# Optimization experiments

Measured on AMD Instinct MI355X. Metric: run time of the kernel, lower is better.

## Reference

```python
import jax, jax.numpy as jnp
import numpy as np

N_NODES = 50000
N_EDGES = 600000
IN_FEATS = 128
N_HIDDEN = 128
N_CLASSES = 40


def setup_inputs() -> dict:
    key = jax.random.key(0)
    ks = jax.random.split(key, 12)
    feat = jax.random.normal(ks[0], (N_NODES, IN_FEATS), dtype=jnp.float32)
    src = jax.random.randint(ks[1], (N_EDGES,), 0, N_NODES, dtype=jnp.int32)
    dst = jax.random.randint(ks[2], (N_EDGES,), 0, N_NODES, dtype=jnp.int32)
    dims = [(IN_FEATS, N_HIDDEN), (N_HIDDEN, N_HIDDEN), (N_HIDDEN, N_CLASSES)]
    params = {}
    for i, (di, do) in enumerate(dims):
        s = 1.0 / np.sqrt(di)
        params[f"w_self{i}"] = jax.random.uniform(ks[3 + 3 * i], (di, do), jnp.float32, -s, s)
        params[f"w_neigh{i}"] = jax.random.uniform(ks[4 + 3 * i], (di, do), jnp.float32, -s, s)
        params[f"b{i}"] = jnp.zeros((do,), jnp.float32)
    return dict(feat=feat, src=src, dst=dst, **params)


def _sage_layer(h, src, dst, w_self, w_neigh, b):
    # mean aggregation over in-neighbors: msg = h[src], reduce at dst
    msg_sum = jax.ops.segment_sum(h[src], dst, num_segments=N_NODES)  # [N, d]
    deg = jax.ops.segment_sum(jnp.ones((src.shape[0],), h.dtype), dst, num_segments=N_NODES)
    h_neigh = msg_sum / jnp.maximum(deg, 1.0)[:, None]
    # DGL SAGEConv(mean): out = fc_self(h) + fc_neigh(mean_neigh) + bias
    return h @ w_self + h_neigh @ w_neigh + b


def reference(feat, src, dst,
              w_self0, w_neigh0, b0,
              w_self1, w_neigh1, b1,
              w_self2, w_neigh2, b2):
    # dropout p=0.0 -> identity
    h = _sage_layer(feat, src, dst, w_self0, w_neigh0, b0)
    h = jax.nn.relu(h)
    h = _sage_layer(h, src, dst, w_self1, w_neigh1, b1)
    h = jax.nn.relu(h)
    h = _sage_layer(h, src, dst, w_self2, w_neigh2, b2)
    return h
```

## Files before the change

### kernel.cpp

```cpp
#include <hip/hip_runtime.h>

#define N_NODES 50000
#define N_EDGES 600000

typedef short bf16x8 __attribute__((ext_vector_type(8)));
typedef float f32x4  __attribute__((ext_vector_type(4)));
typedef unsigned short u16x8 __attribute__((ext_vector_type(8)));
typedef unsigned short u16x4 __attribute__((ext_vector_type(4)));

typedef __attribute__((address_space(1))) unsigned int u32_g;
typedef __attribute__((address_space(3))) unsigned int u32_l;

__device__ inline void g2lds16(const void* g, void* l) {
    __builtin_amdgcn_global_load_lds((const u32_g*)g, (u32_l*)l, 16, 0, 0);
}

__device__ inline ushort rne_bf16(float a) {
    union { float f; unsigned u; } v; v.f = a;
    return (ushort)((v.u + 0x7FFFu + ((v.u >> 16) & 1u)) >> 16);
}
__device__ inline float bf16_to_f32(ushort h) {
    return __uint_as_float((unsigned)h << 16);
}
__device__ inline void split_bf16(float a, ushort& hi, ushort& lo) {
    hi = rne_bf16(a);
    float hv = bf16_to_f32(hi);
    lo = rne_bf16(a - hv);
}


__global__ void count_deg_kernel(const int* __restrict__ dst, int* __restrict__ deg, int ne) {
    int e = blockIdx.x * blockDim.x + threadIdx.x;
    if (e < ne) atomicAdd(&deg[dst[e]], 1);
}

__global__ __launch_bounds__(256) void block_sums_kernel(const int* __restrict__ deg,
                                                         int* __restrict__ bsum, int n) {
    __shared__ int s[256];
    int t = threadIdx.x;
    int i = blockIdx.x * 256 + t;
    s[t] = (i < n) ? deg[i] : 0;
    __syncthreads();
    #pragma unroll
    for (int d = 128; d > 0; d >>= 1) {
        if (t < d) s[t] += s[t + d];
        __syncthreads();
    }
    if (t == 0) bsum[blockIdx.x] = s[0];
}

__global__ __launch_bounds__(256) void scan_bsums_kernel(const int* __restrict__ bsum,
                                                         int* __restrict__ base, int nb,
                                                         int* __restrict__ off, int n) {
    __shared__ int s[256];
    int t = threadIdx.x;
    int v = (t < nb) ? bsum[t] : 0;
    s[t] = v;
    __syncthreads();
    #pragma unroll
    for (int d = 1; d < 256; d <<= 1) {
        int x = (t >= d) ? s[t - d] : 0;
        __syncthreads();
        s[t] += x;
        __syncthreads();
    }
    if (t < nb) base[t] = s[t] - v;
    if (t == 255) off[n] = s[255];
}

__global__ __launch_bounds__(256) void scatter_offsets_kernel(const int* __restrict__ deg,
                                                              const int* __restrict__ base,
                                                              int* __restrict__ off,
                                                              int* __restrict__ cur, int n) {
    __shared__ int s[256];
    int t = threadIdx.x;
    int i = blockIdx.x * 256 + t;
    int v = (i < n) ? deg[i] : 0;
    s[t] = v;
    __syncthreads();
    #pragma unroll
    for (int d = 1; d < 256; d <<= 1) {
        int x = (t >= d) ? s[t - d] : 0;
        __syncthreads();
        s[t] += x;
        __syncthreads();
    }
    if (i < n) {
        int excl = s[t] - v + base[blockIdx.x];
        off[i] = excl;
        cur[i] = excl;
    }
}

__global__ void fill_csr_kernel(const int* __restrict__ src, const int* __restrict__ dst,
                                int* __restrict__ cur, int* __restrict__ ssrc, int ne) {
    int e = blockIdx.x * blockDim.x + threadIdx.x;
    if (e < ne) {
        int p = atomicAdd(&cur[dst[e]], 1);
        ssrc[p] = src[e];
    }
}

__global__ void convert_w_kernel(const float* __restrict__ Ws, const float* __restrict__ Wn,
                                 int dout, ushort* __restrict__ Bth, ushort* __restrict__ Btl) {
    int n = blockIdx.x;
    int k = threadIdx.x;
    float w = (n < dout) ? Ws[(long)k * dout + n] : Wn[(long)k * dout + (n - dout)];
    ushort hi, lo;
    split_bf16(w, hi, lo);
    Bth[n * 128 + k] = hi;
    Btl[n * 128 + k] = lo;
}

__global__ __launch_bounds__(256) void convert_feat_kernel(const float* __restrict__ A,
                                                           ushort* __restrict__ Ah,
                                                           ushort* __restrict__ Al) {
    long g = ((long)blockIdx.x * 256 + threadIdx.x) * 8;
    float4 a0 = *(const float4*)(A + g);
    float4 a1 = *(const float4*)(A + g + 4);
    float f[8] = {a0.x, a0.y, a0.z, a0.w, a1.x, a1.y, a1.z, a1.w};
    u16x8 h, l;
    #pragma unroll
    for (int i = 0; i < 8; ++i) {
        ushort hh, ll;
        split_bf16(f[i], hh, ll);
        h[i] = hh; l[i] = ll;
    }
    *(u16x8*)(Ah + g) = h;
    *(u16x8*)(Al + g) = l;
}


#define KDIM 128
#define TILES 3
#define RPB   (32 * TILES)

__global__ __launch_bounds__(512) void gemm_mfma_wide(
    const ushort* __restrict__ Ah, const ushort* __restrict__ Al,
    const ushort* __restrict__ Bth, const ushort* __restrict__ Btl,
    const float* __restrict__ bias,
    float* __restrict__ S, ushort* __restrict__ T, int M)
{
    __shared__ ushort AhL[32 * 128];
    __shared__ ushort AlL[32 * 128];

    const int tid = threadIdx.x;
    const int wave = tid >> 6;
    const int lane = tid & 63;
    const int lane16 = lane & 15;
    const int quad = lane >> 4;
    const int colbase = wave * 32;
    const int rowbase = blockIdx.x * RPB;

    bf16x8 bh[2][4], bl[2][4];
    #pragma unroll
    for (int ct = 0; ct < 2; ++ct) {
        #pragma unroll
        for (int c = 0; c < 4; ++c) {
            long boff = (long)(colbase + 16 * ct + lane16) * KDIM + c * 32 + quad * 8;
            bh[ct][c] = *(const bf16x8*)(Bth + boff);
            bl[ct][c] = *(const bf16x8*)(Btl + boff);
        }
    }

    const int srow = tid >> 4;
    const int su   = (tid & 15) ^ (srow & 15);
    const int lds_wave_off = wave * 512;

    for (int t = 0; t < TILES; ++t) {
        const int r0 = rowbase + t * 32;
        {
            const ushort* ga = Ah + ((long)(r0 + srow) * KDIM + su * 8);
            const ushort* gb = Al + ((long)(r0 + srow) * KDIM + su * 8);
            g2lds16(ga, (void*)(AhL + lds_wave_off));
            g2lds16(gb, (void*)(AlL + lds_wave_off));
        }
        __syncthreads();

        f32x4 acc[2][2] = {};
        #pragma unroll
        for (int c = 0; c < 4; ++c) {
            bf16x8 ah[2], al[2];
            #pragma unroll
            for (int rt = 0; rt < 2; ++rt) {
                int row = 16 * rt + lane16;
                int u = (4 * c + quad) ^ lane16;
                int offs = row * 128 + u * 8;
                ah[rt] = *(const bf16x8*)&AhL[offs];
                al[rt] = *(const bf16x8*)&AlL[offs];
            }
            #pragma unroll
            for (int ct = 0; ct < 2; ++ct)
                #pragma unroll
                for (int rt = 0; rt < 2; ++rt)
                    acc[rt][ct] = __builtin_amdgcn_mfma_f32_16x16x32_bf16(ah[rt], bh[ct][c], acc[rt][ct], 0, 0, 0);
            #pragma unroll
            for (int ct = 0; ct < 2; ++ct)
                #pragma unroll
                for (int rt = 0; rt < 2; ++rt)
                    acc[rt][ct] = __builtin_amdgcn_mfma_f32_16x16x32_bf16(ah[rt], bl[ct][c], acc[rt][ct], 0, 0, 0);
            #pragma unroll
            for (int ct = 0; ct < 2; ++ct)
                #pragma unroll
                for (int rt = 0; rt < 2; ++rt)
                    acc[rt][ct] = __builtin_amdgcn_mfma_f32_16x16x32_bf16(al[rt], bh[ct][c], acc[rt][ct], 0, 0, 0);
        }

        #pragma unroll
        for (int ct = 0; ct < 2; ++ct) {
            int col = colbase + 16 * ct + lane16;
            bool toS = col < 128;
            float bv = toS ? bias[col] : 0.f;
            int tcol = toS ? col : col - 128;
            #pragma unroll
            for (int rt = 0; rt < 2; ++rt) {
                #pragma unroll
                for (int i = 0; i < 4; ++i) {
                    int row = r0 + 16 * rt + quad * 4 + i;
                    if (row < M) {
                        if (toS) S[(long)row * 128 + tcol] = acc[rt][ct][i] + bv;
                        else     T[(long)row * 128 + tcol] = rne_bf16(acc[rt][ct][i]);
                    }
                }
            }
        }
        __syncthreads();
    }
}

__global__ __launch_bounds__(256) void gemm_mfma_narrow(
    const ushort* __restrict__ Ah, const ushort* __restrict__ Al,
    const ushort* __restrict__ Bth, const ushort* __restrict__ Btl,
    const float* __restrict__ bias,
    float* __restrict__ S, ushort* __restrict__ T, int M)
{
    const int tid = threadIdx.x;
    const int wave = tid >> 6;
    const int brow = blockIdx.x * 64 + wave * 16;
    const int lane = tid & 63;
    const int lane16 = lane & 15;
    const int quad = lane >> 4;

    f32x4 acc[5] = {};

    #pragma unroll
    for (int c = 0; c < 4; ++c) {
        const int k0 = c * 32;
        long aoff = (long)(brow + lane16) * KDIM + k0 + quad * 8;
        bf16x8 ah = *(const bf16x8*)(Ah + aoff);
        bf16x8 al = *(const bf16x8*)(Al + aoff);
        bf16x8 bh[5], bl[5];
        #pragma unroll
        for (int ct = 0; ct < 5; ++ct) {
            long boff = (long)(16 * ct + lane16) * KDIM + k0 + quad * 8;
            bh[ct] = *(const bf16x8*)(Bth + boff);
            bl[ct] = *(const bf16x8*)(Btl + boff);
        }
        #pragma unroll
        for (int ct = 0; ct < 5; ++ct)
            acc[ct] = __builtin_amdgcn_mfma_f32_16x16x32_bf16(ah, bh[ct], acc[ct], 0, 0, 0);
        #pragma unroll
        for (int ct = 0; ct < 5; ++ct)
            acc[ct] = __builtin_amdgcn_mfma_f32_16x16x32_bf16(ah, bl[ct], acc[ct], 0, 0, 0);
        #pragma unroll
        for (int ct = 0; ct < 5; ++ct)
            acc[ct] = __builtin_amdgcn_mfma_f32_16x16x32_bf16(al, bh[ct], acc[ct], 0, 0, 0);
    }

    #pragma unroll
    for (int ct = 0; ct < 5; ++ct) {
        int col = 16 * ct + lane16;
        bool toS = col < 40;
        float bv = toS ? bias[col] : 0.f;
        int tcol = toS ? col : col - 40;
        #pragma unroll
        for (int i = 0; i < 4; ++i) {
            int row = brow + quad * 4 + i;
            if (row < M) {
                if (toS) S[(long)row * 40 + tcol] = acc[ct][i] + bv;
                else     T[(long)row * 40 + tcol] = rne_bf16(acc[ct][i]);
            }
        }
    }
}


__global__ __launch_bounds__(256) void agg128_split_kernel(
    const float* __restrict__ S, const ushort* __restrict__ T,
    const int* __restrict__ off, const int* __restrict__ ssrc,
    ushort* __restrict__ Oh, ushort* __restrict__ Ol, int nnodes)
{
    const int node = (blockIdx.x * 256 + threadIdx.x) >> 6;
    if (node >= nnodes) return;
    const int lane = threadIdx.x & 63;
    const int slot = lane >> 4;
    const int col8 = (lane & 15) * 8;

    const int a = off[node];
    const int b = off[node + 1];

    f32x4 acc0a = {0,0,0,0}, acc0b = {0,0,0,0};
    f32x4 acc1a = {0,0,0,0}, acc1b = {0,0,0,0};

    int i = a;
    for (; i + 8 <= b; i += 8) {
        int s0 = ssrc[i + slot];
        int s1 = ssrc[i + 4 + slot];
        u16x8 v0 = *(const u16x8*)(T + (long)s0 * 128 + col8);
        u16x8 v1 = *(const u16x8*)(T + (long)s1 * 128 + col8);
        #pragma unroll
        for (int j = 0; j < 4; ++j) {
            acc0a[j] += bf16_to_f32(v0[j]);
            acc0b[j] += bf16_to_f32(v0[4 + j]);
            acc1a[j] += bf16_to_f32(v1[j]);
            acc1b[j] += bf16_to_f32(v1[4 + j]);
        }
    }
    for (; i < b; i += 4) {
        int e = i + slot;
        if (e < b) {
            int s = ssrc[e];
            u16x8 v = *(const u16x8*)(T + (long)s * 128 + col8);
            #pragma unroll
            for (int j = 0; j < 4; ++j) {
                acc0a[j] += bf16_to_f32(v[j]);
                acc0b[j] += bf16_to_f32(v[4 + j]);
            }
        }
    }
    f32x4 accA = acc0a + acc1a;
    f32x4 accB = acc0b + acc1b;

    #pragma unroll
    for (int m = 16; m <= 32; m <<= 1) {
        #pragma unroll
        for (int j = 0; j < 4; ++j) {
            accA[j] += __shfl_xor((float)accA[j], m);
            accB[j] += __shfl_xor((float)accB[j], m);
        }
    }

    if (slot == 0) {
        int deg = b - a;
        float scale = (deg > 0) ? (1.0f / (float)deg) : 0.f;
        f32x4 sA = *(const f32x4*)(S + (long)node * 128 + col8);
        f32x4 sB = *(const f32x4*)(S + (long)node * 128 + col8 + 4);
        float r[8];
        #pragma unroll
        for (int j = 0; j < 4; ++j) {
            r[j]     = fmaxf(sA[j] + accA[j] * scale, 0.f);
            r[4 + j] = fmaxf(sB[j] + accB[j] * scale, 0.f);
        }
        u16x8 h, l;
        #pragma unroll
        for (int j = 0; j < 8; ++j) {
            ushort hh, ll;
            split_bf16(r[j], hh, ll);
            h[j] = hh; l[j] = ll;
        }
        *(u16x8*)(Oh + (long)node * 128 + col8) = h;
        *(u16x8*)(Ol + (long)node * 128 + col8) = l;
    }
}

__global__ __launch_bounds__(256) void agg40_kernel(
    const float* __restrict__ S, const ushort* __restrict__ T,
    const int* __restrict__ off, const int* __restrict__ ssrc,
    float* __restrict__ out, int nnodes)
{
    const int node = (blockIdx.x * 256 + threadIdx.x) >> 6;
    if (node >= nnodes) return;
    const int lane = threadIdx.x & 63;
    const bool active = lane < 60;
    const int slot = active ? (lane / 10) : 5;
    const int fi = lane % 10;
    const int fo = fi * 4;

    const int a = off[node];
    const int b = off[node + 1];

    f32x4 acc0 = {0,0,0,0}, acc1 = {0,0,0,0};

    int i = a;
    for (; i + 12 <= b; i += 12) {
        int s0 = ssrc[i + slot];
        int s1 = ssrc[i + 6 + slot];
        u16x4 v0 = *(const u16x4*)(T + (long)s0 * 40 + fo);
        u16x4 v1 = *(const u16x4*)(T + (long)s1 * 40 + fo);
        if (active) {
            #pragma unroll
            for (int j = 0; j < 4; ++j) {
                acc0[j] += bf16_to_f32(v0[j]);
                acc1[j] += bf16_to_f32(v1[j]);
            }
        }
    }
    for (; i < b; i += 6) {
        int e = i + slot;
        if (active && e < b) {
            int s = ssrc[e];
            u16x4 v = *(const u16x4*)(T + (long)s * 40 + fo);
            #pragma unroll
            for (int j = 0; j < 4; ++j) acc0[j] += bf16_to_f32(v[j]);
        }
    }
    f32x4 acc = acc0 + acc1;

    f32x4 tot = acc;
    #pragma unroll
    for (int d = 10; d <= 50; d += 10) {
        int srcl = fi + d;
        #pragma unroll
        for (int j = 0; j < 4; ++j) tot[j] += __shfl((float)acc[j], srcl);
    }

    if (lane < 10) {
        int deg = b - a;
        float scale = (deg > 0) ? (1.0f / (float)deg) : 0.f;
        f32x4 s4 = *(const f32x4*)(S + (long)node * 40 + fo);
        f32x4 r = s4 + tot * scale;
        *(f32x4*)(out + (long)node * 40 + fo) = r;
    }
}


extern "C" void kernel_launch(void* const* d_in, const int* in_sizes, int n_in,
                              void* d_out, int out_size, void* d_ws, size_t ws_size,
                              hipStream_t stream) {
    const float* feat = (const float*)d_in[0];
    const int*   src  = (const int*)d_in[1];
    const int*   dst  = (const int*)d_in[2];
    const float* ws0  = (const float*)d_in[3];
    const float* wn0  = (const float*)d_in[4];
    const float* b0   = (const float*)d_in[5];
    const float* ws1  = (const float*)d_in[6];
    const float* wn1  = (const float*)d_in[7];
    const float* b1   = (const float*)d_in[8];
    const float* ws2  = (const float*)d_in[9];
    const float* wn2  = (const float*)d_in[10];
    const float* b2   = (const float*)d_in[11];

    const int N = N_NODES;
    const int NE = N_EDGES;
    const int NB = (N + 255) / 256;

    char* ws = (char*)d_ws;
    int*    offsets = (int*)(ws + 0);
    int*    cursor  = (int*)(ws + 200704);
    int*    degi    = (int*)(ws + 401408);
    int*    bsum    = (int*)(ws + 601600);
    int*    bbase   = (int*)(ws + 602432);
    int*    ssrc    = (int*)(ws + 603648);
    ushort* Bth0 = (ushort*)(ws + 200704);
    ushort* Btl0 = (ushort*)(ws + 266240);
    ushort* Bth1 = (ushort*)(ws + 331776);
    ushort* Btl1 = (ushort*)(ws + 397312);
    ushort* Bth2 = (ushort*)(ws + 462848);
    ushort* Btl2 = (ushort*)(ws + 483328);
    ushort* fh   = (ushort*)(ws + 3010560);
    ushort* fl   = (ushort*)(ws + 15827200);
    float*  sbuf = (float*)(ws + 28643840);
    ushort* tbuf = (ushort*)(ws + 54244096);

    hipMemsetAsync(degi, 0, (size_t)N * sizeof(int), stream);
    count_deg_kernel<<<(NE + 255) / 256, 256, 0, stream>>>(dst, degi, NE);
    block_sums_kernel<<<NB, 256, 0, stream>>>(degi, bsum, N);
    scan_bsums_kernel<<<1, 256, 0, stream>>>(bsum, bbase, NB, offsets, N);
    scatter_offsets_kernel<<<NB, 256, 0, stream>>>(degi, bbase, offsets, cursor, N);
    fill_csr_kernel<<<(NE + 255) / 256, 256, 0, stream>>>(src, dst, cursor, ssrc, NE);

    convert_w_kernel<<<256, 128, 0, stream>>>(ws0, wn0, 128, Bth0, Btl0);
    convert_w_kernel<<<256, 128, 0, stream>>>(ws1, wn1, 128, Bth1, Btl1);
    convert_w_kernel<<<80, 128, 0, stream>>>(ws2, wn2, 40, Bth2, Btl2);
    convert_feat_kernel<<<(N * 128 / 8 + 255) / 256, 256, 0, stream>>>(feat, fh, fl);

    const int gw = (N + RPB - 1) / RPB;
    const int gn = (N + 63) / 64;
    const int ga = (N + 3) / 4;

    gemm_mfma_wide<<<gw, 512, 0, stream>>>(fh, fl, Bth0, Btl0, b0, sbuf, tbuf, N);
    agg128_split_kernel<<<ga, 256, 0, stream>>>(sbuf, tbuf, offsets, ssrc, fh, fl, N);

    gemm_mfma_wide<<<gw, 512, 0, stream>>>(fh, fl, Bth1, Btl1, b1, sbuf, tbuf, N);
    agg128_split_kernel<<<ga, 256, 0, stream>>>(sbuf, tbuf, offsets, ssrc, fh, fl, N);

    gemm_mfma_narrow<<<gn, 256, 0, stream>>>(fh, fl, Bth2, Btl2, b2, sbuf, tbuf, N);
    agg40_kernel<<<ga, 256, 0, stream>>>(sbuf, tbuf, offsets, ssrc, (float*)d_out, N);
}
```

Baseline: 338.8 us.

## Fuse setup kernels, merge scan passes, double-buffer GEMM tiles, unroll aggregation

Degree counting, feature splitting and weight splitting are merged into one multi-role launch, and the block-sum and scan kernels are combined using a last-block-done counter. The wide GEMM double-buffers its LDS A tiles so the next tile's load overlaps the current MFMA work, and occupancy is hinted through launch bounds. The 128-wide aggregation gathers four neighbor rows per step with more accumulators to raise memory-level parallelism. This trades launch overhead and serialization for more LDS use, more registers, and atomic/fence-based inter-block coordination.

```diff
diff --git a/kernel.cpp b/kernel.cpp
--- a/kernel.cpp
+++ b/kernel.cpp
@@ -28,15 +28,62 @@
     lo = rne_bf16(a - hv);
 }
 
-
-__global__ void count_deg_kernel(const int* __restrict__ dst, int* __restrict__ deg, int ne) {
-    int e = blockIdx.x * blockDim.x + threadIdx.x;
-    if (e < ne) atomicAdd(&deg[dst[e]], 1);
-}
-
-__global__ __launch_bounds__(256) void block_sums_kernel(const int* __restrict__ deg,
-                                                         int* __restrict__ bsum, int n) {
+#define NB_EDGE 2344
+#define NB_FEAT 3125
+#define NB_W01  128
+#define NB_W2   40
+
+__global__ __launch_bounds__(256) void setup_kernel(
+    const int* __restrict__ dst, int* __restrict__ deg,
+    const float* __restrict__ feat, ushort* __restrict__ fh, ushort* __restrict__ fl,
+    const float* __restrict__ Ws0, const float* __restrict__ Wn0, ushort* __restrict__ Bth0, ushort* __restrict__ Btl0,
+    const float* __restrict__ Ws1, const float* __restrict__ Wn1, ushort* __restrict__ Bth1, ushort* __restrict__ Btl1,
+    const float* __restrict__ Ws2, const float* __restrict__ Wn2, ushort* __restrict__ Bth2, ushort* __restrict__ Btl2)
+{
+    const int b = blockIdx.x;
+    const int t = threadIdx.x;
+    if (b < NB_EDGE) {
+        int e = b * 256 + t;
+        if (e < N_EDGES) atomicAdd(&deg[dst[e]], 1);
+    } else if (b < NB_EDGE + NB_FEAT) {
+        long g = ((long)(b - NB_EDGE) * 256 + t) * 8;
+        float4 a0 = *(const float4*)(feat + g);
+        float4 a1 = *(const float4*)(feat + g + 4);
+        float f[8] = {a0.x, a0.y, a0.z, a0.w, a1.x, a1.y, a1.z, a1.w};
+        u16x8 h, l;
+        #pragma unroll
+        for (int i = 0; i < 8; ++i) {
+            ushort hh, ll;
+            split_bf16(f[i], hh, ll);
+            h[i] = hh; l[i] = ll;
+        }
+        *(u16x8*)(fh + g) = h;
+        *(u16x8*)(fl + g) = l;
+    } else {
+        const float* Ws; const float* Wn; ushort* Bh; ushort* Bl; int dout, bb;
+        if (b < NB_EDGE + NB_FEAT + NB_W01) {
+            bb = b - (NB_EDGE + NB_FEAT); Ws = Ws0; Wn = Wn0; Bh = Bth0; Bl = Btl0; dout = 128;
+        } else if (b < NB_EDGE + NB_FEAT + 2 * NB_W01) {
+            bb = b - (NB_EDGE + NB_FEAT + NB_W01); Ws = Ws1; Wn = Wn1; Bh = Bth1; Bl = Btl1; dout = 128;
+        } else {
+            bb = b - (NB_EDGE + NB_FEAT + 2 * NB_W01); Ws = Ws2; Wn = Wn2; Bh = Bth2; Bl = Btl2; dout = 40;
+        }
+        int n = 2 * bb + (t >> 7);
+        int k = t & 127;
+        float w = (n < dout) ? Ws[(long)k * dout + n] : Wn[(long)k * dout + (n - dout)];
+        ushort hi, lo;
+        split_bf16(w, hi, lo);
+        Bh[n * 128 + k] = hi;
+        Bl[n * 128 + k] = lo;
+    }
+}
+
+__global__ __launch_bounds__(256) void block_sums_scan_kernel(
+    const int* __restrict__ deg, int* __restrict__ bsum, int* __restrict__ counter,
+    int* __restrict__ base, int* __restrict__ off, int n, int nb)
+{
     __shared__ int s[256];
+    __shared__ int amLast;
     int t = threadIdx.x;
     int i = blockIdx.x * 256 + t;
     s[t] = (i < n) ? deg[i] : 0;
@@ -46,26 +93,27 @@
         if (t < d) s[t] += s[t + d];
         __syncthreads();
     }
-    if (t == 0) bsum[blockIdx.x] = s[0];
-}
-
-__global__ __launch_bounds__(256) void scan_bsums_kernel(const int* __restrict__ bsum,
-                                                         int* __restrict__ base, int nb,
-                                                         int* __restrict__ off, int n) {
-    __shared__ int s[256];
-    int t = threadIdx.x;
-    int v = (t < nb) ? bsum[t] : 0;
-    s[t] = v;
+    if (t == 0) {
+        atomicExch(&bsum[blockIdx.x], s[0]);
+        __threadfence();
+        int prev = atomicAdd(counter, 1);
+        amLast = (prev == nb - 1) ? 1 : 0;
+    }
     __syncthreads();
-    #pragma unroll
-    for (int d = 1; d < 256; d <<= 1) {
-        int x = (t >= d) ? s[t - d] : 0;
+    if (amLast) {
+        int v = (t < nb) ? atomicAdd(&bsum[t], 0) : 0;
+        s[t] = v;
         __syncthreads();
-        s[t] += x;
-        __syncthreads();
-    }
-    if (t < nb) base[t] = s[t] - v;
-    if (t == 255) off[n] = s[255];
+        #pragma unroll
+        for (int d = 1; d < 256; d <<= 1) {
+            int x = (t >= d) ? s[t - d] : 0;
+            __syncthreads();
+            s[t] += x;
+            __syncthreads();
+        }
+        if (t < nb) base[t] = s[t] - v;
+        if (t == 255) off[n] = s[255];
+    }
 }
 
 __global__ __launch_bounds__(256) void scatter_offsets_kernel(const int* __restrict__ deg,
@@ -101,48 +149,19 @@
     }
 }
 
-__global__ void convert_w_kernel(const float* __restrict__ Ws, const float* __restrict__ Wn,
-                                 int dout, ushort* __restrict__ Bth, ushort* __restrict__ Btl) {
-    int n = blockIdx.x;
-    int k = threadIdx.x;
-    float w = (n < dout) ? Ws[(long)k * dout + n] : Wn[(long)k * dout + (n - dout)];
-    ushort hi, lo;
-    split_bf16(w, hi, lo);
-    Bth[n * 128 + k] = hi;
-    Btl[n * 128 + k] = lo;
-}
-
-__global__ __launch_bounds__(256) void convert_feat_kernel(const float* __restrict__ A,
-                                                           ushort* __restrict__ Ah,
-                                                           ushort* __restrict__ Al) {
-    long g = ((long)blockIdx.x * 256 + threadIdx.x) * 8;
-    float4 a0 = *(const float4*)(A + g);
-    float4 a1 = *(const float4*)(A + g + 4);
-    float f[8] = {a0.x, a0.y, a0.z, a0.w, a1.x, a1.y, a1.z, a1.w};
-    u16x8 h, l;
-    #pragma unroll
-    for (int i = 0; i < 8; ++i) {
-        ushort hh, ll;
-        split_bf16(f[i], hh, ll);
-        h[i] = hh; l[i] = ll;
-    }
-    *(u16x8*)(Ah + g) = h;
-    *(u16x8*)(Al + g) = l;
-}
-
 
 #define KDIM 128
 #define TILES 3
 #define RPB   (32 * TILES)
 
-__global__ __launch_bounds__(512) void gemm_mfma_wide(
+__global__ __launch_bounds__(512, 4) void gemm_mfma_wide(
     const ushort* __restrict__ Ah, const ushort* __restrict__ Al,
     const ushort* __restrict__ Bth, const ushort* __restrict__ Btl,
     const float* __restrict__ bias,
     float* __restrict__ S, ushort* __restrict__ T, int M)
 {
-    __shared__ ushort AhL[32 * 128];
-    __shared__ ushort AlL[32 * 128];
+    __shared__ ushort AhL[2][32 * 128];
+    __shared__ ushort AlL[2][32 * 128];
 
     const int tid = threadIdx.x;
     const int wave = tid >> 6;
@@ -167,15 +186,25 @@
     const int su   = (tid & 15) ^ (srow & 15);
     const int lds_wave_off = wave * 512;
 
+    {
+        const ushort* ga = Ah + ((long)(rowbase + srow) * KDIM + su * 8);
+        const ushort* gb = Al + ((long)(rowbase + srow) * KDIM + su * 8);
+        g2lds16(ga, (void*)(&AhL[0][lds_wave_off]));
+        g2lds16(gb, (void*)(&AlL[0][lds_wave_off]));
+    }
+
+    int cur = 0;
     for (int t = 0; t < TILES; ++t) {
         const int r0 = rowbase + t * 32;
-        {
-            const ushort* ga = Ah + ((long)(r0 + srow) * KDIM + su * 8);
-            const ushort* gb = Al + ((long)(r0 + srow) * KDIM + su * 8);
-            g2lds16(ga, (void*)(AhL + lds_wave_off));
-            g2lds16(gb, (void*)(AlL + lds_wave_off));
-        }
         __syncthreads();
+
+        if (t + 1 < TILES) {
+            const int rn = r0 + 32;
+            const ushort* ga = Ah + ((long)(rn + srow) * KDIM + su * 8);
+            const ushort* gb = Al + ((long)(rn + srow) * KDIM + su * 8);
+            g2lds16(ga, (void*)(&AhL[cur ^ 1][lds_wave_off]));
+            g2lds16(gb, (void*)(&AlL[cur ^ 1][lds_wave_off]));
+        }
 
         f32x4 acc[2][2] = {};
         #pragma unroll
@@ -186,8 +215,8 @@
                 int row = 16 * rt + lane16;
                 int u = (4 * c + quad) ^ lane16;
                 int offs = row * 128 + u * 8;
-                ah[rt] = *(const bf16x8*)&AhL[offs];
-                al[rt] = *(const bf16x8*)&AlL[offs];
+                ah[rt] = *(const bf16x8*)&AhL[cur][offs];
+                al[rt] = *(const bf16x8*)&AlL[cur][offs];
             }
             #pragma unroll
             for (int ct = 0; ct < 2; ++ct)
@@ -224,7 +253,7 @@
                 }
             }
         }
-        __syncthreads();
+        cur ^= 1;
     }
 }
 
@@ -299,21 +328,34 @@
     const int a = off[node];
     const int b = off[node + 1];
 
-    f32x4 acc0a = {0,0,0,0}, acc0b = {0,0,0,0};
-    f32x4 acc1a = {0,0,0,0}, acc1b = {0,0,0,0};
+    f32x4 aA[4] = {{0,0,0,0},{0,0,0,0},{0,0,0,0},{0,0,0,0}};
+    f32x4 aB[4] = {{0,0,0,0},{0,0,0,0},{0,0,0,0},{0,0,0,0}};
 
     int i = a;
-    for (; i + 8 <= b; i += 8) {
+    for (; i + 16 <= b; i += 16) {
         int s0 = ssrc[i + slot];
         int s1 = ssrc[i + 4 + slot];
+        int s2 = ssrc[i + 8 + slot];
+        int s3 = ssrc[i + 12 + slot];
         u16x8 v0 = *(const u16x8*)(T + (long)s0 * 128 + col8);
         u16x8 v1 = *(const u16x8*)(T + (long)s1 * 128 + col8);
+        u16x8 v2 = *(const u16x8*)(T + (long)s2 * 128 + col8);
+        u16x8 v3 = *(const u16x8*)(T + (long)s3 * 128 + col8);
         #pragma unroll
         for (int j = 0; j < 4; ++j) {
-            acc0a[j] += bf16_to_f32(v0[j]);
-            acc0b[j] += bf16_to_f32(v0[4 + j]);
-            acc1a[j] += bf16_to_f32(v1[j]);
-            acc1b[j] += bf16_to_f32(v1[4 + j]);
+            aA[0][j] += bf16_to_f32(v0[j]);  aB[0][j] += bf16_to_f32(v0[4 + j]);
+            aA[1][j] += bf16_to_f32(v1[j]);  aB[1][j] += bf16_to_f32(v1[4 + j]);
+            aA[2][j] += bf16_to_f32(v2[j]);  aB[2][j] += bf16_to_f32(v2[4 + j]);
+            aA[3][j] += bf16_to_f32(v3[j]);  aB[3][j] += bf16_to_f32(v3[4 + j]);
+        }
+    }
+    for (; i + 4 <= b; i += 4) {
+        int s0 = ssrc[i + slot];
+        u16x8 v = *(const u16x8*)(T + (long)s0 * 128 + col8);
+        #pragma unroll
+        for (int j = 0; j < 4; ++j) {
+            aA[0][j] += bf16_to_f32(v[j]);
+            aB[0][j] += bf16_to_f32(v[4 + j]);
         }
     }
     for (; i < b; i += 4) {
@@ -323,13 +365,13 @@
             u16x8 v = *(const u16x8*)(T + (long)s * 128 + col8);
             #pragma unroll
             for (int j = 0; j < 4; ++j) {
-                acc0a[j] += bf16_to_f32(v[j]);
-                acc0b[j] += bf16_to_f32(v[4 + j]);
+                aA[1][j] += bf16_to_f32(v[j]);
+                aB[1][j] += bf16_to_f32(v[4 + j]);
             }
         }
     }
-    f32x4 accA = acc0a + acc1a;
-    f32x4 accB = acc0b + acc1b;
+    f32x4 accA = (aA[0] + aA[1]) + (aA[2] + aA[3]);
+    f32x4 accB = (aB[0] + aB[1]) + (aB[2] + aB[3]);
 
     #pragma unroll
     for (int m = 16; m <= 32; m <<= 1) {
@@ -448,31 +490,32 @@
     int*    offsets = (int*)(ws + 0);
     int*    cursor  = (int*)(ws + 200704);
     int*    degi    = (int*)(ws + 401408);
+    int*    counter = (int*)(ws + 601408);
     int*    bsum    = (int*)(ws + 601600);
     int*    bbase   = (int*)(ws + 602432);
     int*    ssrc    = (int*)(ws + 603648);
-    ushort* Bth0 = (ushort*)(ws + 200704);
-    ushort* Btl0 = (ushort*)(ws + 266240);
-    ushort* Bth1 = (ushort*)(ws + 331776);
-    ushort* Btl1 = (ushort*)(ws + 397312);
-    ushort* Bth2 = (ushort*)(ws + 462848);
-    ushort* Btl2 = (ushort*)(ws + 483328);
-    ushort* fh   = (ushort*)(ws + 3010560);
-    ushort* fl   = (ushort*)(ws + 15827200);
-    float*  sbuf = (float*)(ws + 28643840);
-    ushort* tbuf = (ushort*)(ws + 54244096);
-
-    hipMemsetAsync(degi, 0, (size_t)N * sizeof(int), stream);
-    count_deg_kernel<<<(NE + 255) / 256, 256, 0, stream>>>(dst, degi, NE);
-    block_sums_kernel<<<NB, 256, 0, stream>>>(degi, bsum, N);
-    scan_bsums_kernel<<<1, 256, 0, stream>>>(bsum, bbase, NB, offsets, N);
+    ushort* Bth0 = (ushort*)(ws + 3003904);
+    ushort* Btl0 = (ushort*)(ws + 3069440);
+    ushort* Bth1 = (ushort*)(ws + 3134976);
+    ushort* Btl1 = (ushort*)(ws + 3200512);
+    ushort* Bth2 = (ushort*)(ws + 3266048);
+    ushort* Btl2 = (ushort*)(ws + 3286528);
+    ushort* fh   = (ushort*)(ws + 3307264);
+    ushort* fl   = (ushort*)(ws + 16123904);
+    float*  sbuf = (float*)(ws + 28940544);
+    ushort* tbuf = (ushort*)(ws + 54540800);
+
+    hipMemsetAsync(degi, 0, (size_t)N * sizeof(int) + sizeof(int), stream);
+
+    setup_kernel<<<NB_EDGE + NB_FEAT + 2 * NB_W01 + NB_W2, 256, 0, stream>>>(
+        dst, degi, feat, fh, fl,
+        ws0, wn0, Bth0, Btl0,
+        ws1, wn1, Bth1, Btl1,
+        ws2, wn2, Bth2, Btl2);
+
+    block_sums_scan_kernel<<<NB, 256, 0, stream>>>(degi, bsum, counter, bbase, offsets, N, NB);
     scatter_offsets_kernel<<<NB, 256, 0, stream>>>(degi, bbase, offsets, cursor, N);
     fill_csr_kernel<<<(NE + 255) / 256, 256, 0, stream>>>(src, dst, cursor, ssrc, NE);
-
-    convert_w_kernel<<<256, 128, 0, stream>>>(ws0, wn0, 128, Bth0, Btl0);
-    convert_w_kernel<<<256, 128, 0, stream>>>(ws1, wn1, 128, Bth1, Btl1);
-    convert_w_kernel<<<80, 128, 0, stream>>>(ws2, wn2, 40, Bth2, Btl2);
-    convert_feat_kernel<<<(N * 128 / 8 + 255) / 256, 256, 0, stream>>>(feat, fh, fl);
 
     const int gw = (N + RPB - 1) / RPB;
     const int gn = (N + 63) / 64;
```

Result: slower. 347.5 us (+2.6%).
